# Optimization experiments

Measured on AMD Instinct MI355X. Metric: run time of the kernel, lower is better.

## Reference

```python
import jax, jax.numpy as jnp
import numpy as np

EPS = 1e-6


def setup_inputs() -> dict:
    key = jax.random.key(0)
    kx, kp = jax.random.split(key)
    B, D, P = 16384, 1024, 1024
    x = jax.random.normal(kx, (B, D), dtype=jnp.float32)
    prototypes = jax.random.normal(kp, (P, D), dtype=jnp.float32)
    return {"x": x, "prototypes": prototypes}


def reference(x, prototypes):
    # Vectorized form of the per-(sample, prototype) yat similarity:
    #   score[i, j] = <x_i, p_j>^2 / (||x_i - p_j||^2 + eps)
    # x: [B, D], prototypes: [P, D] -> scores: [B, P]
    x_flat = x.reshape(x.shape[0], -1)
    dots = jnp.einsum("bd,pd->bp", x_flat, prototypes)          # [B, P] GEMM
    x_sq = jnp.sum(x_flat * x_flat, axis=-1, keepdims=True)      # [B, 1]
    p_sq = jnp.sum(prototypes * prototypes, axis=-1)[None, :]    # [1, P]
    dist_sq = x_sq + p_sq - 2.0 * dots                            # ||x - p||^2
    scores = (dots * dots) / (dist_sq + EPS)
    return scores.astype(jnp.float32)
```

## Files before the change

kernel.cpp:

```cpp
#include <hip/hip_runtime.h>
#include <hip/hip_bf16.h>

#define EPS 1e-6f

typedef __attribute__((ext_vector_type(8))) __bf16 bf16x8;
typedef __attribute__((ext_vector_type(4))) float f32x4;

__global__ __launch_bounds__(512, 2) void yat_fused(
    const float* __restrict__ X, const float* __restrict__ Pr,
    float* __restrict__ out, int M, int N, int K) {

    __shared__ __align__(128) char sm[131072];
    __shared__ __align__(16) float sqx[256];
    __shared__ __align__(16) float sqp[256];
    const char* smc = (const char*)sm;

    const int t = threadIdx.x;
    const int lane = t & 63;
    const int wid = t >> 6;
    const int wm = wid >> 2;
    const int wn = wid & 3;

    const int nbx = N >> 8;
    const int nby = M >> 8;
    const int total = nbx * nby;
    int bid = blockIdx.x;
    bid = (bid & 7) * (total >> 3) + (bid >> 3);
    const int by = bid / nbx;
    const int bx = bid - by * nbx;
    const int brow = by << 8;
    const int bcol = bx << 8;

    const int NKT = K >> 6;

    f32x4 acc[8][4];
#pragma unroll
    for (int i = 0; i < 8; ++i)
#pragma unroll
        for (int j = 0; j < 4; ++j) acc[i][j] = (f32x4){0.f, 0.f, 0.f, 0.f};

    const int arow = lane & 15;
    const int kq16 = (lane >> 4) * 16;

    const int rsub = lane >> 3;
    const int lcq = (lane & 7) ^ rsub;
    const long baseA = (long)(brow + wid * 8 + rsub) * K + lcq * 8;
    const long baseB = (long)(bcol + wid * 8 + rsub) * K + lcq * 8;
    const long sH = (long)128 * K, sL = (long)64 * K;
    const int dlane = wid * 1024 + lane * 16;

    f32x4 c0[2], c1[2];
    float qA[2][2] = {{0.f, 0.f}, {0.f, 0.f}};
    float qB[2][2] = {{0.f, 0.f}, {0.f, 0.f}};

#define ISSUE(buf, G, BASE, hh, l, kt) do {                                    \
    const float* g0_ = (G) + BASE + (hh) * sH + (l) * sL + (long)(kt) * 64;    \
    buf[0] = *(const f32x4*)(g0_);                                             \
    buf[1] = *(const f32x4*)(g0_ + 4);                                         \
} while (0)

#define WRITE(buf, Q, hh, l, slot, boff) do {                                  \
    f32x4 u_ = buf[0], v_ = buf[1];                                            \
    Q[hh][l] += u_[0]*u_[0] + u_[1]*u_[1] + u_[2]*u_[2] + u_[3]*u_[3]          \
              + v_[0]*v_[0] + v_[1]*v_[1] + v_[2]*v_[2] + v_[3]*v_[3];         \
    bf16x8 pk_;                                                                \
    _Pragma("unroll")                                                          \
    for (int i_ = 0; i_ < 4; ++i_) {                                           \
        pk_[i_]     = (__bf16)u_[i_];                                          \
        pk_[4 + i_] = (__bf16)v_[i_];                                          \
    }                                                                          \
    *(bf16x8*)((char*)sm + (slot) * 65536 + (boff) + (hh) * 16384              \
               + (l) * 8192 + dlane) = pk_;                                    \
} while (0)

#define READ_A(slot, mh) do {                                                  \
    _Pragma("unroll")                                                          \
    for (int mi_ = 0; mi_ < 4; ++mi_) {                                        \
        int r_ = wm * 128 + (mh) * 64 + mi_ * 16 + arow;                       \
        const char* p_ = smc + (slot) * 65536 + r_ * 128;                      \
        int s_ = (r_ & 7) << 4;                                                \
        af[mi_][0] = *(const bf16x8*)(p_ + (kq16 ^ s_));                       \
        af[mi_][1] = *(const bf16x8*)(p_ + ((64 + kq16) ^ s_));                \
    }                                                                          \
} while (0)

#define READ_B(slot, nh, dst) do {                                             \
    _Pragma("unroll")                                                          \
    for (int ni_ = 0; ni_ < 2; ++ni_) {                                        \
        int r_ = wn * 64 + (nh) * 32 + ni_ * 16 + arow;                        \
        const char* p_ = smc + (slot) * 65536 + 32768 + r_ * 128;              \
        int s_ = (r_ & 7) << 4;                                                \
        dst[ni_][0] = *(const bf16x8*)(p_ + (kq16 ^ s_));                      \
        dst[ni_][1] = *(const bf16x8*)(p_ + ((64 + kq16) ^ s_));               \
    }                                                                          \
} while (0)

#define MFMA_Q(mh, nh, bset) do {                                              \
    __builtin_amdgcn_s_setprio(1);                                             \
    _Pragma("unroll")                                                          \
    for (int kk_ = 0; kk_ < 2; ++kk_)                                          \
        _Pragma("unroll")                                                      \
        for (int mi_ = 0; mi_ < 4; ++mi_)                                      \
            _Pragma("unroll")                                                  \
            for (int ni_ = 0; ni_ < 2; ++ni_)                                  \
                acc[(mh) * 4 + mi_][(nh) * 2 + ni_] =                          \
                    __builtin_amdgcn_mfma_f32_16x16x32_bf16(                   \
                        af[mi_][kk_], bset[ni_][kk_],                          \
                        acc[(mh) * 4 + mi_][(nh) * 2 + ni_], 0, 0, 0);         \
    __builtin_amdgcn_s_setprio(0);                                             \
} while (0)

#define PBAR() do {                                                            \
    __builtin_amdgcn_s_barrier();                                              \
    __builtin_amdgcn_sched_barrier(0);                                         \
    asm volatile("" ::: "memory");                                             \
} while (0)
#define LGKMDRAIN() asm volatile("s_waitcnt lgkmcnt(0)" ::: "memory")

    bf16x8 af[4][2];
    bf16x8 bf0[2][2], bf1[2][2];

    ISSUE(c0, X, baseA, 0, 0, 0);
    ISSUE(c1, X, baseA, 0, 1, 0);
    WRITE(c0, qA, 0, 0, 0, 0);  ISSUE(c0, X, baseA, 1, 0, 0);
    WRITE(c1, qA, 0, 1, 0, 0);  ISSUE(c1, X, baseA, 1, 1, 0);
    WRITE(c0, qA, 1, 0, 0, 0);  ISSUE(c0, Pr, baseB, 0, 0, 0);
    WRITE(c1, qA, 1, 1, 0, 0);  ISSUE(c1, Pr, baseB, 0, 1, 0);
    WRITE(c0, qB, 0, 0, 0, 32768);  ISSUE(c0, Pr, baseB, 1, 0, 0);
    WRITE(c1, qB, 0, 1, 0, 32768);  ISSUE(c1, Pr, baseB, 1, 1, 0);
    WRITE(c0, qB, 1, 0, 0, 32768);
    WRITE(c1, qB, 1, 1, 0, 32768);
    if (NKT > 1) { ISSUE(c0, X, baseA, 0, 0, 1); ISSUE(c1, X, baseA, 0, 1, 1); }
    LGKMDRAIN();
    PBAR();

    for (int kt = 0; kt < NKT; ++kt) {
        const int slot = kt & 1;
        const int nslot = slot ^ 1;
        const bool more = (kt + 1) < NKT;
        const bool more2 = (kt + 2) < NKT;

        if (more) {
            WRITE(c0, qA, 0, 0, nslot, 0);  ISSUE(c0, X, baseA, 1, 0, kt + 1);
            WRITE(c1, qA, 0, 1, nslot, 0);  ISSUE(c1, X, baseA, 1, 1, kt + 1);
        }
        READ_A(slot, 0); READ_B(slot, 0, bf0);
        MFMA_Q(0, 0, bf0); PBAR();
        if (more) {
            WRITE(c0, qA, 1, 0, nslot, 0);  ISSUE(c0, Pr, baseB, 0, 0, kt + 1);
            WRITE(c1, qA, 1, 1, nslot, 0);  ISSUE(c1, Pr, baseB, 0, 1, kt + 1);
        }
        READ_B(slot, 1, bf1);
        MFMA_Q(0, 1, bf1); PBAR();
        if (more) {
            WRITE(c0, qB, 0, 0, nslot, 32768);  ISSUE(c0, Pr, baseB, 1, 0, kt + 1);
            WRITE(c1, qB, 0, 1, nslot, 32768);  ISSUE(c1, Pr, baseB, 1, 1, kt + 1);
        }
        READ_A(slot, 1);
        MFMA_Q(1, 0, bf0); PBAR();
        if (more) {
            WRITE(c0, qB, 1, 0, nslot, 32768);
            WRITE(c1, qB, 1, 1, nslot, 32768);
        }
        if (more2) { ISSUE(c0, X, baseA, 0, 0, kt + 2); ISSUE(c1, X, baseA, 0, 1, kt + 2); }
        MFMA_Q(1, 1, bf1);
        LGKMDRAIN();
        PBAR();
    }

#undef ISSUE
#undef WRITE
#undef READ_A
#undef READ_B
#undef MFMA_Q
#undef PBAR
#undef LGKMDRAIN

#pragma unroll
    for (int hh = 0; hh < 2; ++hh)
#pragma unroll
        for (int l = 0; l < 2; ++l) {
            float a = qA[hh][l], b = qB[hh][l];
#pragma unroll
            for (int m = 1; m <= 4; m <<= 1) {
                a += __shfl_xor(a, m);
                b += __shfl_xor(b, m);
            }
            if ((lane & 7) == 0) {
                int r = hh * 128 + l * 64 + wid * 8 + rsub;
                sqx[r] = a;
                sqp[r] = b;
            }
        }

    float* smf = (float*)sm;
#pragma unroll
    for (int pass = 0; pass < 2; ++pass) {
        __syncthreads();
        if (wm == pass) {
#pragma unroll
            for (int ni = 0; ni < 4; ++ni) {
                int lcc = wn * 64 + ni * 16 + arow;
                float ps = sqp[lcc];
#pragma unroll
                for (int mi = 0; mi < 8; ++mi) {
                    f32x4 c = acc[mi][ni];
                    int lr0 = mi * 16 + (lane >> 4) * 4;
                    f32x4 xs4 = *(const f32x4*)(&sqx[pass * 128 + lr0]);
                    int lcs = lcc ^ (((lr0 >> 2) & 1) << 4);
#pragma unroll
                    for (int j = 0; j < 4; ++j) {
                        float dv = c[j];
                        float denom = xs4[j] + ps - 2.0f * dv + EPS;
                        smf[(lr0 + j) * 256 + lcs] = dv * dv / denom;
                    }
                }
            }
        }
        __syncthreads();
#pragma unroll
        for (int rr = 0; rr < 16; ++rr) {
            int r = wid * 16 + rr;
            int swz = ((r >> 2) & 1) << 4;
            int c0l = lane * 4;
            f32x4 v = *(const f32x4*)(smf + r * 256 + (c0l ^ swz));
            *(f32x4*)(out + (size_t)(brow + pass * 128 + r) * N + bcol + c0l) = v;
        }
    }
}

__global__ void yat_fallback(const float* __restrict__ x, const float* __restrict__ p,
                             float* __restrict__ out, int B, int P, int D) {
    __shared__ float xs[1024];
    int b = blockIdx.x;
    int pc = blockIdx.y * 256 + threadIdx.x;
    for (int i = threadIdx.x; i < D; i += 256) xs[i] = x[(size_t)b * D + i];
    __syncthreads();
    if (pc >= P) return;
    float dot = 0.f, psq = 0.f, xsq = 0.f;
    for (int k = 0; k < D; ++k) {
        float pv = p[(size_t)pc * D + k];
        float xv = xs[k];
        dot += xv * pv;
        psq += pv * pv;
        xsq += xv * xv;
    }
    float denom = xsq + psq - 2.f * dot + EPS;
    out[(size_t)b * P + pc] = dot * dot / denom;
}

extern "C" void kernel_launch(void* const* d_in, const int* in_sizes, int n_in,
                              void* d_out, int out_size, void* d_ws, size_t ws_size,
                              hipStream_t stream) {
    const float* x = (const float*)d_in[0];
    const float* p = (const float*)d_in[1];
    float* out = (float*)d_out;

    const int D = 1024;
    const int B = in_sizes[0] / D;
    const int P = in_sizes[1] / D;

    int nblocks = (B / 256) * (P / 256);
    if ((B % 256) || (P % 256) || (D % 64) || (nblocks % 8)) {
        yat_fallback<<<dim3(B, (P + 255) / 256), 256, 0, stream>>>(x, p, out, B, P, D);
        return;
    }

    yat_fused<<<dim3(nblocks), 512, 0, stream>>>(x, p, out, B, P, D);
}
```

Before: 66.09 us.

## Shrink fused yat GEMM tile to 128x128 with higher occupancy

Reduces each block's output tile from 256x256 to 128x128, halving shared memory and accumulator registers. The warp layout becomes 4x2 waves with 32x64 subtiles, and the k-loop pipeline is simplified to two MFMA phases. The aim is more blocks and better latency hiding and load balance across CUs, at the cost of lower operand reuse and more global traffic for re-reading and converting X and P.

```diff
diff --git a/kernel.cpp b/kernel.cpp
--- a/kernel.cpp
+++ b/kernel.cpp
@@ -6,36 +6,36 @@
 typedef __attribute__((ext_vector_type(8))) __bf16 bf16x8;
 typedef __attribute__((ext_vector_type(4))) float f32x4;
 
-__global__ __launch_bounds__(512, 2) void yat_fused(
+__global__ __launch_bounds__(512, 4) void yat_fused(
     const float* __restrict__ X, const float* __restrict__ Pr,
     float* __restrict__ out, int M, int N, int K) {
 
-    __shared__ __align__(128) char sm[131072];
-    __shared__ __align__(16) float sqx[256];
-    __shared__ __align__(16) float sqp[256];
+    __shared__ __align__(128) char sm[65536];
+    __shared__ __align__(16) float sqx[128];
+    __shared__ __align__(16) float sqp[128];
     const char* smc = (const char*)sm;
 
     const int t = threadIdx.x;
     const int lane = t & 63;
     const int wid = t >> 6;
-    const int wm = wid >> 2;
-    const int wn = wid & 3;
-
-    const int nbx = N >> 8;
-    const int nby = M >> 8;
+    const int wm = wid >> 1;
+    const int wn = wid & 1;
+
+    const int nbx = N >> 7;
+    const int nby = M >> 7;
     const int total = nbx * nby;
     int bid = blockIdx.x;
     bid = (bid & 7) * (total >> 3) + (bid >> 3);
     const int by = bid / nbx;
     const int bx = bid - by * nbx;
-    const int brow = by << 8;
-    const int bcol = bx << 8;
+    const int brow = by << 7;
+    const int bcol = bx << 7;
 
     const int NKT = K >> 6;
 
-    f32x4 acc[8][4];
-#pragma unroll
-    for (int i = 0; i < 8; ++i)
+    f32x4 acc[2][4];
+#pragma unroll
+    for (int i = 0; i < 2; ++i)
 #pragma unroll
         for (int j = 0; j < 4; ++j) acc[i][j] = (f32x4){0.f, 0.f, 0.f, 0.f};
 
@@ -46,38 +46,37 @@
     const int lcq = (lane & 7) ^ rsub;
     const long baseA = (long)(brow + wid * 8 + rsub) * K + lcq * 8;
     const long baseB = (long)(bcol + wid * 8 + rsub) * K + lcq * 8;
-    const long sH = (long)128 * K, sL = (long)64 * K;
+    const long sL = (long)64 * K;
     const int dlane = wid * 1024 + lane * 16;
 
     f32x4 c0[2], c1[2];
-    float qA[2][2] = {{0.f, 0.f}, {0.f, 0.f}};
-    float qB[2][2] = {{0.f, 0.f}, {0.f, 0.f}};
-
-#define ISSUE(buf, G, BASE, hh, l, kt) do {                                    \
-    const float* g0_ = (G) + BASE + (hh) * sH + (l) * sL + (long)(kt) * 64;    \
+    float qA[2] = {0.f, 0.f};
+    float qB[2] = {0.f, 0.f};
+
+#define ISSUE(buf, G, BASE, s, kt) do {                                        \
+    const float* g0_ = (G) + BASE + (s) * sL + (long)(kt) * 64;                \
     buf[0] = *(const f32x4*)(g0_);                                             \
     buf[1] = *(const f32x4*)(g0_ + 4);                                         \
 } while (0)
 
-#define WRITE(buf, Q, hh, l, slot, boff) do {                                  \
+#define WRITE(buf, Q, s, slot, boff) do {                                      \
     f32x4 u_ = buf[0], v_ = buf[1];                                            \
-    Q[hh][l] += u_[0]*u_[0] + u_[1]*u_[1] + u_[2]*u_[2] + u_[3]*u_[3]          \
-              + v_[0]*v_[0] + v_[1]*v_[1] + v_[2]*v_[2] + v_[3]*v_[3];         \
+    Q[s] += u_[0]*u_[0] + u_[1]*u_[1] + u_[2]*u_[2] + u_[3]*u_[3]              \
+          + v_[0]*v_[0] + v_[1]*v_[1] + v_[2]*v_[2] + v_[3]*v_[3];             \
     bf16x8 pk_;                                                                \
     _Pragma("unroll")                                                          \
     for (int i_ = 0; i_ < 4; ++i_) {                                           \
         pk_[i_]     = (__bf16)u_[i_];                                          \
         pk_[4 + i_] = (__bf16)v_[i_];                                          \
     }                                                                          \
-    *(bf16x8*)((char*)sm + (slot) * 65536 + (boff) + (hh) * 16384              \
-               + (l) * 8192 + dlane) = pk_;                                    \
-} while (0)
-
-#define READ_A(slot, mh) do {                                                  \
-    _Pragma("unroll")                                                          \
-    for (int mi_ = 0; mi_ < 4; ++mi_) {                                        \
-        int r_ = wm * 128 + (mh) * 64 + mi_ * 16 + arow;                       \
-        const char* p_ = smc + (slot) * 65536 + r_ * 128;                      \
+    *(bf16x8*)((char*)sm + (slot) * 32768 + (boff) + (s) * 8192 + dlane) = pk_;\
+} while (0)
+
+#define READ_A(slot) do {                                                      \
+    _Pragma("unroll")                                                          \
+    for (int mi_ = 0; mi_ < 2; ++mi_) {                                        \
+        int r_ = wm * 32 + mi_ * 16 + arow;                                    \
+        const char* p_ = smc + (slot) * 32768 + r_ * 128;                      \
         int s_ = (r_ & 7) << 4;                                                \
         af[mi_][0] = *(const bf16x8*)(p_ + (kq16 ^ s_));                       \
         af[mi_][1] = *(const bf16x8*)(p_ + ((64 + kq16) ^ s_));                \
@@ -88,25 +87,25 @@
     _Pragma("unroll")                                                          \
     for (int ni_ = 0; ni_ < 2; ++ni_) {                                        \
         int r_ = wn * 64 + (nh) * 32 + ni_ * 16 + arow;                        \
-        const char* p_ = smc + (slot) * 65536 + 32768 + r_ * 128;              \
+        const char* p_ = smc + (slot) * 32768 + 16384 + r_ * 128;              \
         int s_ = (r_ & 7) << 4;                                                \
         dst[ni_][0] = *(const bf16x8*)(p_ + (kq16 ^ s_));                      \
         dst[ni_][1] = *(const bf16x8*)(p_ + ((64 + kq16) ^ s_));               \
     }                                                                          \
 } while (0)
 
-#define MFMA_Q(mh, nh, bset) do {                                              \
+#define MFMA_H(nh, bset) do {                                                  \
     __builtin_amdgcn_s_setprio(1);                                             \
     _Pragma("unroll")                                                          \
     for (int kk_ = 0; kk_ < 2; ++kk_)                                          \
         _Pragma("unroll")                                                      \
-        for (int mi_ = 0; mi_ < 4; ++mi_)                                      \
+        for (int mi_ = 0; mi_ < 2; ++mi_)                                      \
             _Pragma("unroll")                                                  \
             for (int ni_ = 0; ni_ < 2; ++ni_)                                  \
-                acc[(mh) * 4 + mi_][(nh) * 2 + ni_] =                          \
+                acc[mi_][(nh) * 2 + ni_] =                                     \
                     __builtin_amdgcn_mfma_f32_16x16x32_bf16(                   \
                         af[mi_][kk_], bset[ni_][kk_],                          \
-                        acc[(mh) * 4 + mi_][(nh) * 2 + ni_], 0, 0, 0);         \
+                        acc[mi_][(nh) * 2 + ni_], 0, 0, 0);                    \
     __builtin_amdgcn_s_setprio(0);                                             \
 } while (0)
 
@@ -117,20 +116,16 @@
 } while (0)
 #define LGKMDRAIN() asm volatile("s_waitcnt lgkmcnt(0)" ::: "memory")
 
-    bf16x8 af[4][2];
+    bf16x8 af[2][2];
     bf16x8 bf0[2][2], bf1[2][2];
 
-    ISSUE(c0, X, baseA, 0, 0, 0);
-    ISSUE(c1, X, baseA, 0, 1, 0);
-    WRITE(c0, qA, 0, 0, 0, 0);  ISSUE(c0, X, baseA, 1, 0, 0);
-    WRITE(c1, qA, 0, 1, 0, 0);  ISSUE(c1, X, baseA, 1, 1, 0);
-    WRITE(c0, qA, 1, 0, 0, 0);  ISSUE(c0, Pr, baseB, 0, 0, 0);
-    WRITE(c1, qA, 1, 1, 0, 0);  ISSUE(c1, Pr, baseB, 0, 1, 0);
-    WRITE(c0, qB, 0, 0, 0, 32768);  ISSUE(c0, Pr, baseB, 1, 0, 0);
-    WRITE(c1, qB, 0, 1, 0, 32768);  ISSUE(c1, Pr, baseB, 1, 1, 0);
-    WRITE(c0, qB, 1, 0, 0, 32768);
-    WRITE(c1, qB, 1, 1, 0, 32768);
-    if (NKT > 1) { ISSUE(c0, X, baseA, 0, 0, 1); ISSUE(c1, X, baseA, 0, 1, 1); }
+    ISSUE(c0, X, baseA, 0, 0);
+    ISSUE(c1, X, baseA, 1, 0);
+    WRITE(c0, qA, 0, 0, 0);       ISSUE(c0, Pr, baseB, 0, 0);
+    WRITE(c1, qA, 1, 0, 0);       ISSUE(c1, Pr, baseB, 1, 0);
+    WRITE(c0, qB, 0, 0, 16384);
+    WRITE(c1, qB, 1, 0, 16384);
+    if (NKT > 1) { ISSUE(c0, X, baseA, 0, 1); ISSUE(c1, X, baseA, 1, 1); }
     LGKMDRAIN();
     PBAR();
 
@@ -141,29 +136,18 @@
         const bool more2 = (kt + 2) < NKT;
 
         if (more) {
-            WRITE(c0, qA, 0, 0, nslot, 0);  ISSUE(c0, X, baseA, 1, 0, kt + 1);
-            WRITE(c1, qA, 0, 1, nslot, 0);  ISSUE(c1, X, baseA, 1, 1, kt + 1);
-        }
-        READ_A(slot, 0); READ_B(slot, 0, bf0);
-        MFMA_Q(0, 0, bf0); PBAR();
+            WRITE(c0, qA, 0, nslot, 0);      ISSUE(c0, Pr, baseB, 0, kt + 1);
+            WRITE(c1, qA, 1, nslot, 0);      ISSUE(c1, Pr, baseB, 1, kt + 1);
+        }
+        READ_A(slot); READ_B(slot, 0, bf0);
+        MFMA_H(0, bf0); PBAR();
         if (more) {
-            WRITE(c0, qA, 1, 0, nslot, 0);  ISSUE(c0, Pr, baseB, 0, 0, kt + 1);
-            WRITE(c1, qA, 1, 1, nslot, 0);  ISSUE(c1, Pr, baseB, 0, 1, kt + 1);
-        }
+            WRITE(c0, qB, 0, nslot, 16384);
+            WRITE(c1, qB, 1, nslot, 16384);
+        }
+        if (more2) { ISSUE(c0, X, baseA, 0, kt + 2); ISSUE(c1, X, baseA, 1, kt + 2); }
         READ_B(slot, 1, bf1);
-        MFMA_Q(0, 1, bf1); PBAR();
-        if (more) {
-            WRITE(c0, qB, 0, 0, nslot, 32768);  ISSUE(c0, Pr, baseB, 1, 0, kt + 1);
-            WRITE(c1, qB, 0, 1, nslot, 32768);  ISSUE(c1, Pr, baseB, 1, 1, kt + 1);
-        }
-        READ_A(slot, 1);
-        MFMA_Q(1, 0, bf0); PBAR();
-        if (more) {
-            WRITE(c0, qB, 1, 0, nslot, 32768);
-            WRITE(c1, qB, 1, 1, nslot, 32768);
-        }
-        if (more2) { ISSUE(c0, X, baseA, 0, 0, kt + 2); ISSUE(c1, X, baseA, 0, 1, kt + 2); }
-        MFMA_Q(1, 1, bf1);
+        MFMA_H(1, bf1);
         LGKMDRAIN();
         PBAR();
     }
@@ -172,60 +156,53 @@
 #undef WRITE
 #undef READ_A
 #undef READ_B
-#undef MFMA_Q
+#undef MFMA_H
 #undef PBAR
 #undef LGKMDRAIN
 
 #pragma unroll
-    for (int hh = 0; hh < 2; ++hh)
-#pragma unroll
-        for (int l = 0; l < 2; ++l) {
-            float a = qA[hh][l], b = qB[hh][l];
-#pragma unroll
-            for (int m = 1; m <= 4; m <<= 1) {
-                a += __shfl_xor(a, m);
-                b += __shfl_xor(b, m);
+    for (int s = 0; s < 2; ++s) {
+        float a = qA[s], b = qB[s];
+#pragma unroll
+        for (int m = 1; m <= 4; m <<= 1) {
+            a += __shfl_xor(a, m);
+            b += __shfl_xor(b, m);
+        }
+        if ((lane & 7) == 0) {
+            int r = s * 64 + wid * 8 + rsub;
+            sqx[r] = a;
+            sqp[r] = b;
+        }
+    }
+    __syncthreads();
+
+    float* smf = (float*)sm;
+#pragma unroll
+    for (int ni = 0; ni < 4; ++ni) {
+        int lcc = wn * 64 + ni * 16 + arow;
+        float ps = sqp[lcc];
+#pragma unroll
+        for (int mi = 0; mi < 2; ++mi) {
+            f32x4 c = acc[mi][ni];
+            int lr0 = wm * 32 + mi * 16 + (lane >> 4) * 4;
+            f32x4 xs4 = *(const f32x4*)(&sqx[lr0]);
+            int lcs = lcc ^ (((lr0 >> 2) & 1) << 4);
+#pragma unroll
+            for (int j = 0; j < 4; ++j) {
+                float dv = c[j];
+                float denom = xs4[j] + ps - 2.0f * dv + EPS;
+                smf[(lr0 + j) * 128 + lcs] = dv * dv / denom;
             }
-            if ((lane & 7) == 0) {
-                int r = hh * 128 + l * 64 + wid * 8 + rsub;
-                sqx[r] = a;
-                sqp[r] = b;
-            }
-        }
-
-    float* smf = (float*)sm;
-#pragma unroll
-    for (int pass = 0; pass < 2; ++pass) {
-        __syncthreads();
-        if (wm == pass) {
-#pragma unroll
-            for (int ni = 0; ni < 4; ++ni) {
-                int lcc = wn * 64 + ni * 16 + arow;
-                float ps = sqp[lcc];
-#pragma unroll
-                for (int mi = 0; mi < 8; ++mi) {
-                    f32x4 c = acc[mi][ni];
-                    int lr0 = mi * 16 + (lane >> 4) * 4;
-                    f32x4 xs4 = *(const f32x4*)(&sqx[pass * 128 + lr0]);
-                    int lcs = lcc ^ (((lr0 >> 2) & 1) << 4);
-#pragma unroll
-                    for (int j = 0; j < 4; ++j) {
-                        float dv = c[j];
-                        float denom = xs4[j] + ps - 2.0f * dv + EPS;
-                        smf[(lr0 + j) * 256 + lcs] = dv * dv / denom;
-                    }
-                }
-            }
-        }
-        __syncthreads();
-#pragma unroll
-        for (int rr = 0; rr < 16; ++rr) {
-            int r = wid * 16 + rr;
-            int swz = ((r >> 2) & 1) << 4;
-            int c0l = lane * 4;
-            f32x4 v = *(const f32x4*)(smf + r * 256 + (c0l ^ swz));
-            *(f32x4*)(out + (size_t)(brow + pass * 128 + r) * N + bcol + c0l) = v;
-        }
+        }
+    }
+    __syncthreads();
+#pragma unroll
+    for (int it = 0; it < 8; ++it) {
+        int r = it * 16 + (t >> 5);
+        int swz = ((r >> 2) & 1) << 4;
+        int c0l = (t & 31) * 4;
+        f32x4 v = *(const f32x4*)(smf + r * 128 + (c0l ^ swz));
+        *(f32x4*)(out + (size_t)(brow + r) * N + bcol + c0l) = v;
     }
 }
 
@@ -260,8 +237,8 @@
     const int B = in_sizes[0] / D;
     const int P = in_sizes[1] / D;
 
-    int nblocks = (B / 256) * (P / 256);
-    if ((B % 256) || (P % 256) || (D % 64) || (nblocks % 8)) {
+    int nblocks = (B / 128) * (P / 128);
+    if ((B % 128) || (P % 128) || (D % 64) || (nblocks % 8)) {
         yat_fallback<<<dim3(B, (P + 255) / 256), 256, 0, stream>>>(x, p, out, B, P, D);
         return;
     }
```

Result: slower. 72.34 us (+9.5%).

## Pre-convert prototypes to bf16 and stream them into LDS via global_load_lds

Applied to the files above, without the earlier changes.

A small prep kernel converts the prototype matrix to bf16 once and computes its row squared norms into the workspace. The fused GEMM then loads B tiles straight from global memory into LDS with global_load_lds, skipping the per-block fp32 load, convert and LDS write, and reads precomputed norms instead of accumulating them. The X loads are regrouped into one wider batch per k-tile with an explicit vmcnt wait. The cost is an extra kernel launch and a dependence on workspace size, and the new prefetch schedule and wait counts must stay consistent to avoid races.

```diff
diff --git a/kernel.cpp b/kernel.cpp
--- a/kernel.cpp
+++ b/kernel.cpp
@@ -6,13 +6,47 @@
 typedef __attribute__((ext_vector_type(8))) __bf16 bf16x8;
 typedef __attribute__((ext_vector_type(4))) float f32x4;
 
+__device__ inline unsigned short f2bf_rtne(float f) {
+    unsigned int u = __float_as_uint(f);
+    unsigned int r = (u + 0x7FFFu + ((u >> 16) & 1u)) >> 16;
+    return (unsigned short)r;
+}
+
+__global__ void p_prep(const float* __restrict__ in,
+                       unsigned short* __restrict__ hi,
+                       float* __restrict__ sq, int R, int D) {
+    int wid = (blockIdx.x * blockDim.x + threadIdx.x) >> 6;
+    int lane = threadIdx.x & 63;
+    if (wid >= R) return;
+    const float4* rp = (const float4*)(in + (size_t)wid * D);
+    ushort4* hp = (ushort4*)(hi + (size_t)wid * D);
+    float s = 0.f;
+    int nvec = D >> 2;
+    for (int j = lane; j < nvec; j += 64) {
+        float4 v = rp[j];
+        float fv[4] = {v.x, v.y, v.z, v.w};
+        ushort4 h4;
+        unsigned short* hh = (unsigned short*)&h4;
+#pragma unroll
+        for (int i = 0; i < 4; ++i) {
+            float f = fv[i];
+            s += f * f;
+            hh[i] = f2bf_rtne(f);
+        }
+        hp[j] = h4;
+    }
+#pragma unroll
+    for (int off = 32; off; off >>= 1) s += __shfl_down(s, off);
+    if (lane == 0) sq[wid] = s;
+}
+
 __global__ __launch_bounds__(512, 2) void yat_fused(
-    const float* __restrict__ X, const float* __restrict__ Pr,
-    float* __restrict__ out, int M, int N, int K) {
+    const float* __restrict__ X, const unsigned short* __restrict__ Phi,
+    const float* __restrict__ psq, float* __restrict__ out,
+    int M, int N, int K) {
 
     __shared__ __align__(128) char sm[131072];
     __shared__ __align__(16) float sqx[256];
-    __shared__ __align__(16) float sqp[256];
     const char* smc = (const char*)sm;
 
     const int t = threadIdx.x;
@@ -45,32 +79,52 @@
     const int rsub = lane >> 3;
     const int lcq = (lane & 7) ^ rsub;
     const long baseA = (long)(brow + wid * 8 + rsub) * K + lcq * 8;
-    const long baseB = (long)(bcol + wid * 8 + rsub) * K + lcq * 8;
     const long sH = (long)128 * K, sL = (long)64 * K;
     const int dlane = wid * 1024 + lane * 16;
-
-    f32x4 c0[2], c1[2];
+    const size_t rowB = (size_t)K * 2;
+    const int stgc = ((lane & 7) ^ rsub) << 4;
+
+    f32x4 c0[4], c1[4];
     float qA[2][2] = {{0.f, 0.f}, {0.f, 0.f}};
-    float qB[2][2] = {{0.f, 0.f}, {0.f, 0.f}};
-
-#define ISSUE(buf, G, BASE, hh, l, kt) do {                                    \
-    const float* g0_ = (G) + BASE + (hh) * sH + (l) * sL + (long)(kt) * 64;    \
-    buf[0] = *(const f32x4*)(g0_);                                             \
-    buf[1] = *(const f32x4*)(g0_ + 4);                                         \
-} while (0)
-
-#define WRITE(buf, Q, hh, l, slot, boff) do {                                  \
-    f32x4 u_ = buf[0], v_ = buf[1];                                            \
-    Q[hh][l] += u_[0]*u_[0] + u_[1]*u_[1] + u_[2]*u_[2] + u_[3]*u_[3]          \
-              + v_[0]*v_[0] + v_[1]*v_[1] + v_[2]*v_[2] + v_[3]*v_[3];         \
-    bf16x8 pk_;                                                                \
-    _Pragma("unroll")                                                          \
-    for (int i_ = 0; i_ < 4; ++i_) {                                           \
-        pk_[i_]     = (__bf16)u_[i_];                                          \
-        pk_[4 + i_] = (__bf16)v_[i_];                                          \
+
+#define ISSUE_A(kt) do {                                                       \
+    const float* g_ = X + baseA + (long)(kt) * 64;                             \
+    c0[0] = *(const f32x4*)(g_);            c0[1] = *(const f32x4*)(g_ + 4);   \
+    c0[2] = *(const f32x4*)(g_ + sL);       c0[3] = *(const f32x4*)(g_ + sL + 4);\
+    c1[0] = *(const f32x4*)(g_ + sH);       c1[1] = *(const f32x4*)(g_ + sH + 4);\
+    c1[2] = *(const f32x4*)(g_ + sH + sL);  c1[3] = *(const f32x4*)(g_ + sH + sL + 4);\
+} while (0)
+
+#define WRITE_C(buf, hh, slot) do {                                            \
+    _Pragma("unroll")                                                          \
+    for (int l_ = 0; l_ < 2; ++l_) {                                           \
+        f32x4 u_ = buf[2 * l_], v_ = buf[2 * l_ + 1];                          \
+        qA[hh][l_] += u_[0]*u_[0] + u_[1]*u_[1] + u_[2]*u_[2] + u_[3]*u_[3]    \
+                    + v_[0]*v_[0] + v_[1]*v_[1] + v_[2]*v_[2] + v_[3]*v_[3];   \
+        bf16x8 pk_;                                                            \
+        _Pragma("unroll")                                                      \
+        for (int i_ = 0; i_ < 4; ++i_) {                                       \
+            pk_[i_]     = (__bf16)u_[i_];                                      \
+            pk_[4 + i_] = (__bf16)v_[i_];                                      \
+        }                                                                      \
+        *(bf16x8*)((char*)sm + (slot) * 65536 + (hh) * 16384 + l_ * 8192       \
+                   + dlane) = pk_;                                             \
     }                                                                          \
-    *(bf16x8*)((char*)sm + (slot) * 65536 + (boff) + (hh) * 16384              \
-               + (l) * 8192 + dlane) = pk_;                                    \
+} while (0)
+
+#define STAGE_B(kt) do {                                                       \
+    const size_t k0b_ = (size_t)(kt) << 7;                  \
+    char* lb_ = (char*)sm + ((kt) & 1) * 65536 + 32768;                        \
+    _Pragma("unroll")                                                          \
+    for (int l_ = 0; l_ < 4; ++l_) {                                           \
+        int rl_ = (l_ * 8 + wid) * 8 + rsub;                                   \
+        const char* src_ = (const char*)Phi + (size_t)(bcol + rl_) * rowB      \
+                           + k0b_ + stgc;                                      \
+        __builtin_amdgcn_global_load_lds(                                      \
+            (const __attribute__((address_space(1))) void*)src_,               \
+            (__attribute__((address_space(3))) void*)(lb_ + (l_ * 8 + wid) * 1024),\
+            16, 0, 0);                                                         \
+    }                                                                          \
 } while (0)
 
 #define READ_A(slot, mh) do {                                                  \
@@ -116,21 +170,18 @@
     asm volatile("" ::: "memory");                                             \
 } while (0)
 #define LGKMDRAIN() asm volatile("s_waitcnt lgkmcnt(0)" ::: "memory")
+#define VMCNT(n) asm volatile("s_waitcnt vmcnt(" #n ")" ::: "memory")
 
     bf16x8 af[4][2];
     bf16x8 bf0[2][2], bf1[2][2];
 
-    ISSUE(c0, X, baseA, 0, 0, 0);
-    ISSUE(c1, X, baseA, 0, 1, 0);
-    WRITE(c0, qA, 0, 0, 0, 0);  ISSUE(c0, X, baseA, 1, 0, 0);
-    WRITE(c1, qA, 0, 1, 0, 0);  ISSUE(c1, X, baseA, 1, 1, 0);
-    WRITE(c0, qA, 1, 0, 0, 0);  ISSUE(c0, Pr, baseB, 0, 0, 0);
-    WRITE(c1, qA, 1, 1, 0, 0);  ISSUE(c1, Pr, baseB, 0, 1, 0);
-    WRITE(c0, qB, 0, 0, 0, 32768);  ISSUE(c0, Pr, baseB, 1, 0, 0);
-    WRITE(c1, qB, 0, 1, 0, 32768);  ISSUE(c1, Pr, baseB, 1, 1, 0);
-    WRITE(c0, qB, 1, 0, 0, 32768);
-    WRITE(c1, qB, 1, 1, 0, 32768);
-    if (NKT > 1) { ISSUE(c0, X, baseA, 0, 0, 1); ISSUE(c1, X, baseA, 0, 1, 1); }
+    ISSUE_A(0);
+    WRITE_C(c0, 0, 0);
+    WRITE_C(c1, 1, 0);
+    STAGE_B(0);
+    STAGE_B(1);
+    ISSUE_A(1);
+    VMCNT(8);
     LGKMDRAIN();
     PBAR();
 
@@ -140,57 +191,38 @@
         const bool more = (kt + 1) < NKT;
         const bool more2 = (kt + 2) < NKT;
 
-        if (more) {
-            WRITE(c0, qA, 0, 0, nslot, 0);  ISSUE(c0, X, baseA, 1, 0, kt + 1);
-            WRITE(c1, qA, 0, 1, nslot, 0);  ISSUE(c1, X, baseA, 1, 1, kt + 1);
-        }
+        if (more) WRITE_C(c0, 0, nslot);
         READ_A(slot, 0); READ_B(slot, 0, bf0);
         MFMA_Q(0, 0, bf0); PBAR();
-        if (more) {
-            WRITE(c0, qA, 1, 0, nslot, 0);  ISSUE(c0, Pr, baseB, 0, 0, kt + 1);
-            WRITE(c1, qA, 1, 1, nslot, 0);  ISSUE(c1, Pr, baseB, 0, 1, kt + 1);
-        }
+        if (more) WRITE_C(c1, 1, nslot);
         READ_B(slot, 1, bf1);
         MFMA_Q(0, 1, bf1); PBAR();
-        if (more) {
-            WRITE(c0, qB, 0, 0, nslot, 32768);  ISSUE(c0, Pr, baseB, 1, 0, kt + 1);
-            WRITE(c1, qB, 0, 1, nslot, 32768);  ISSUE(c1, Pr, baseB, 1, 1, kt + 1);
-        }
+        if (more2) { STAGE_B(kt + 2); ISSUE_A(kt + 2); }
         READ_A(slot, 1);
         MFMA_Q(1, 0, bf0); PBAR();
-        if (more) {
-            WRITE(c0, qB, 1, 0, nslot, 32768);
-            WRITE(c1, qB, 1, 1, nslot, 32768);
-        }
-        if (more2) { ISSUE(c0, X, baseA, 0, 0, kt + 2); ISSUE(c1, X, baseA, 0, 1, kt + 2); }
         MFMA_Q(1, 1, bf1);
         LGKMDRAIN();
         PBAR();
     }
 
-#undef ISSUE
-#undef WRITE
+#undef ISSUE_A
+#undef WRITE_C
+#undef STAGE_B
 #undef READ_A
 #undef READ_B
 #undef MFMA_Q
 #undef PBAR
 #undef LGKMDRAIN
+#undef VMCNT
 
 #pragma unroll
     for (int hh = 0; hh < 2; ++hh)
 #pragma unroll
         for (int l = 0; l < 2; ++l) {
-            float a = qA[hh][l], b = qB[hh][l];
-#pragma unroll
-            for (int m = 1; m <= 4; m <<= 1) {
-                a += __shfl_xor(a, m);
-                b += __shfl_xor(b, m);
-            }
-            if ((lane & 7) == 0) {
-                int r = hh * 128 + l * 64 + wid * 8 + rsub;
-                sqx[r] = a;
-                sqp[r] = b;
-            }
+            float a = qA[hh][l];
+#pragma unroll
+            for (int m = 1; m <= 4; m <<= 1) a += __shfl_xor(a, m);
+            if ((lane & 7) == 0) sqx[hh * 128 + l * 64 + wid * 8 + rsub] = a;
         }
 
     float* smf = (float*)sm;
@@ -201,7 +233,7 @@
 #pragma unroll
             for (int ni = 0; ni < 4; ++ni) {
                 int lcc = wn * 64 + ni * 16 + arow;
-                float ps = sqp[lcc];
+                float ps = psq[bcol + lcc];
 #pragma unroll
                 for (int mi = 0; mi < 8; ++mi) {
                     f32x4 c = acc[mi][ni];
@@ -260,11 +292,16 @@
     const int B = in_sizes[0] / D;
     const int P = in_sizes[1] / D;
 
+    size_t need = (size_t)P * D * 2 + (size_t)P * 4;
     int nblocks = (B / 256) * (P / 256);
-    if ((B % 256) || (P % 256) || (D % 64) || (nblocks % 8)) {
+    if (ws_size < need || (B % 256) || (P % 256) || (D % 64) || (nblocks % 8)) {
         yat_fallback<<<dim3(B, (P + 255) / 256), 256, 0, stream>>>(x, p, out, B, P, D);
         return;
     }
 
-    yat_fused<<<dim3(nblocks), 512, 0, stream>>>(x, p, out, B, P, D);
-}
+    unsigned short* phi = (unsigned short*)d_ws;
+    float* psq = (float*)(phi + (size_t)P * D);
+
+    p_prep<<<(P + 3) / 4, 256, 0, stream>>>(p, phi, psq, P, D);
+    yat_fused<<<dim3(nblocks), 512, 0, stream>>>(x, phi, psq, out, B, P, D);
+}
```

Result: slower. 82.29 us (+24.5%).
